# Optimization experiments

Hardware: AMD Instinct MI355X
Metric: run time of the kernel (lower is better)

## Reference

```python
import jax, jax.numpy as jnp
import numpy as np

N_MSB = 4      # bit planes
WB = 8         # weight quant bits
ABNM = 8       # activation quant bits (non-MVM)
NL = 0.1       # noise level


def quant(x, bits, r):
    # quant_pass: symmetric round-to-grid inside [-r, r]
    s = 2.0 ** (bits - 1)
    xs = jnp.clip(x / r, -1.0 + 1.0 / s, 1.0 - 1.0 / s)
    return jnp.round(xs * s) / s * r


def pact(x, a):
    # pact_a reduces to a hard clip to [-a, a]
    return jnp.clip(x, -a, a)


def bitsplit(x, n_msb):
    # x in [0,1] -> n_msb binary planes y[i] and beta weights l2/l1
    l1 = 2.0 ** n_msb - 1.0
    l2 = 2.0 ** (n_msb - 1 - jnp.arange(n_msb, dtype=x.dtype))  # [n_msb]
    y = jnp.floor(jnp.round(l1 * x)[None] / l2[:, None, None]) % 2.0  # [n_msb,B,D]
    return y, l2 / l1


def noisy_bmm(inp, W, b, key):
    # CustomMM_bmm.forward: quantized weights + additive gaussian noise
    kw, kb = jax.random.split(key)
    nw = jax.lax.stop_gradient(jax.random.normal(kw, W.shape, W.dtype) * W.max() * NL)
    nb = jax.lax.stop_gradient(jax.random.normal(kb, b.shape, b.dtype) * b.max() * NL)
    wq = quant(W, WB, 1.0)
    bq = quant(b, WB, 1.0)
    return jnp.einsum('mbi,mio->mbo', inp, wq + nw) + bq + nb  # [n_msb,B,4H]


def setup_inputs() -> dict:
    key = jax.random.key(0)
    ks = jax.random.split(key, 9)
    B, I, H, M = 4096, 256, 1024, N_MSB
    inp = {
        'input': jax.random.normal(ks[0], (B, I), jnp.float32),
        'hx': jax.random.normal(ks[1], (B, H), jnp.float32),
        'cx': jax.random.normal(ks[2], (B, H), jnp.float32),
        'weight_ih': jax.random.normal(ks[3], (M, I, 4 * H), jnp.float32),
        'weight_hh': jax.random.normal(ks[4], (M, H, 4 * H), jnp.float32),
        'bias_ih': jax.random.normal(ks[5], (M, 1, 4 * H), jnp.float32),
        'bias_hh': jax.random.normal(ks[6], (M, 1, 4 * H), jnp.float32),
        'a1': jnp.array([128.0], jnp.float32),
        'a3': jnp.array([1.0], jnp.float32),
        'a4': jnp.array([1.0], jnp.float32),
        'a5': jnp.array([1.0], jnp.float32),
        'a6': jnp.array([1.0], jnp.float32),
        'a7': jnp.array([4.0], jnp.float32),
        'a8': jnp.array([1.0], jnp.float32),
        'a9': jnp.array([4.0], jnp.float32),
        'a10': jnp.array([1.0], jnp.float32),
        'a11': jnp.array([4.0], jnp.float32),
    }
    return inp


def reference(input, hx, cx, weight_ih, weight_hh, bias_ih, bias_hh,
              a1, a3, a4, a5, a6, a7, a8, a9, a10, a11):
    k1, k2 = jax.random.split(jax.random.key(42))
    # input branch: clip -> map to [0,1] -> bit-split -> noisy bmm -> threshold -> beta-sum
    inp01 = (pact(input, a1) + a1) / (a1 * 2)
    y, beta = bitsplit(inp01, N_MSB)
    out = (noisy_bmm(y, weight_ih, bias_ih, k1) > 0.5).astype(input.dtype)
    part1 = (beta[:, None, None] * out).sum(0) * (a1 * 2) - a1
    # hidden branch (note: '+ a1' offset as in the original source)
    inp01 = (pact(hx, a11) + a1) / (a11 * 2)
    y, beta = bitsplit(inp01, N_MSB)
    out = (noisy_bmm(y, weight_hh, bias_hh, k2) > 0.5).astype(input.dtype)
    part2 = (beta[:, None, None] * out).sum(0) * (a11 * 2) - a11
    gates = part1 + part2  # [B, 4H]
    i, j, f, o = jnp.split(gates, 4, axis=1)
    fg = quant(pact(jax.nn.sigmoid(f), a3), ABNM, a3)
    ig = quant(pact(jax.nn.sigmoid(i), a4), ABNM, a4)
    act = quant(pact(jnp.tanh(j), a5), ABNM, a5)
    og = quant(pact(jax.nn.sigmoid(o), a6), ABNM, a6)
    gated_cell = quant(pact(cx * fg, a7), ABNM, a7)
    activated_input = quant(pact(ig * act, a8), ABNM, a8)
    new_c = quant(pact(gated_cell + activated_input, a9), ABNM, a9)
    activated_cell = quant(pact(jnp.tanh(new_c), a10), ABNM, a10)
    new_h = quant(pact(activated_cell * og, a11), ABNM, a11)
    return new_h, new_c
```

## Files before the change

### kernel.cpp

```cpp
#include <hip/hip_runtime.h>
#include <cstdint>
#include <cstddef>


typedef int v4i __attribute__((ext_vector_type(4)));

struct KPc { uint32_t a, b; };

__host__ __device__ constexpr KPc ctf(uint32_t k0, uint32_t k1v, uint32_t c0, uint32_t c1) {
  uint32_t ks2 = k0 ^ k1v ^ 0x1BD11BDAu;
  uint32_t x0 = c0 + k0;
  uint32_t x1 = c1 + k1v;
  uint32_t r0[4] = {13u, 15u, 26u, 6u};
  uint32_t r1[4] = {17u, 29u, 16u, 24u};
  uint32_t ks[3] = {k0, k1v, ks2};
  for (int g = 0; g < 5; ++g) {
    for (int j = 0; j < 4; ++j) {
      uint32_t rr = (g & 1) ? r1[j] : r0[j];
      x0 += x1;
      x1 = (x1 << rr) | (x1 >> (32u - rr));
      x1 ^= x0;
    }
    x0 += ks[(g + 1) % 3];
    x1 += ks[(g + 2) % 3] + (uint32_t)(g + 1);
  }
  return KPc{x0, x1};
}

constexpr KPc K1K  = ctf(0u, 42u, 0u, 0u);
constexpr KPc K2K  = ctf(0u, 42u, 0u, 1u);
constexpr KPc KWIH = ctf(K1K.a, K1K.b, 0u, 0u);
constexpr KPc KBIH = ctf(K1K.a, K1K.b, 0u, 1u);
constexpr KPc KWHH = ctf(K2K.a, K2K.b, 0u, 0u);
constexpr KPc KBHH = ctf(K2K.a, K2K.b, 0u, 1u);

__device__ __forceinline__ uint32_t tf_bits(uint32_t k0, uint32_t k1v, uint32_t j) {
  KPc r = ctf(k0, k1v, 0u, j);
  return r.a ^ r.b;
}

__device__ __forceinline__ unsigned encf(float f) {
  unsigned u = __float_as_uint(f);
  return (u & 0x80000000u) ? ~u : (u | 0x80000000u);
}
__device__ __forceinline__ float decf(unsigned e) {
  unsigned u = (e & 0x80000000u) ? (e & 0x7FFFFFFFu) : ~e;
  return __uint_as_float(u);
}

__global__ void rmax_kernel(const float* __restrict__ x, int n, unsigned* __restrict__ out) {
  unsigned best = 0u;
  for (int i = blockIdx.x * blockDim.x + threadIdx.x; i < n; i += gridDim.x * blockDim.x) {
    unsigned e = encf(x[i]);
    best = best > e ? best : e;
  }
  for (int off = 32; off > 0; off >>= 1) {
    unsigned o = __shfl_down(best, off, 64);
    best = best > o ? best : o;
  }
  __shared__ unsigned sm[4];
  int lane = threadIdx.x & 63, wv = threadIdx.x >> 6;
  if (lane == 0) sm[wv] = best;
  __syncthreads();
  if (threadIdx.x == 0) {
    unsigned b = sm[0];
    for (int i = 1; i < 4; ++i) b = b > sm[i] ? b : sm[i];
    atomicMax(out, b);
  }
}

__device__ __forceinline__ float xla_log1p(float t) {
  float small = __fmul_rn(__fadd_rn(__fmul_rn(-0.5f, t), 1.0f), t);
  float large = logf(__fadd_rn(t, 1.0f));
  return (fabsf(t) < 1e-4f) ? small : large;
}

__device__ __forceinline__ float xla_erfinv(float x) {
  float w = -xla_log1p(-__fmul_rn(x, x));
  float p;
  if (w < 5.0f) {
    float ww = __fadd_rn(w, -2.5f);
    p = 2.81022636e-08f;
    p = __fadd_rn(3.43273939e-07f, __fmul_rn(p, ww));
    p = __fadd_rn(-3.5233877e-06f, __fmul_rn(p, ww));
    p = __fadd_rn(-4.39150654e-06f, __fmul_rn(p, ww));
    p = __fadd_rn(0.00021858087f, __fmul_rn(p, ww));
    p = __fadd_rn(-0.00125372503f, __fmul_rn(p, ww));
    p = __fadd_rn(-0.00417768164f, __fmul_rn(p, ww));
    p = __fadd_rn(0.246640727f, __fmul_rn(p, ww));
    p = __fadd_rn(1.50140941f, __fmul_rn(p, ww));
  } else {
    float ww = __fadd_rn(sqrtf(w), -3.0f);
    p = -0.000200214257f;
    p = __fadd_rn(0.000100950558f, __fmul_rn(p, ww));
    p = __fadd_rn(0.00134934322f, __fmul_rn(p, ww));
    p = __fadd_rn(-0.00367342844f, __fmul_rn(p, ww));
    p = __fadd_rn(0.00573950773f, __fmul_rn(p, ww));
    p = __fadd_rn(-0.0076224613f, __fmul_rn(p, ww));
    p = __fadd_rn(0.00943887047f, __fmul_rn(p, ww));
    p = __fadd_rn(1.00167406f, __fmul_rn(p, ww));
    p = __fadd_rn(2.83297682f, __fmul_rn(p, ww));
  }
  return __fmul_rn(p, x);
}

__device__ __forceinline__ float normal_from_bits(uint32_t bits) {
  float u01 = __uint_as_float((bits >> 9) | 0x3f800000u) - 1.0f;
  const float lo = -0x1.fffffep-1f;
  float u = fmaxf(lo, __fadd_rn(__fmul_rn(u01, 2.0f), lo));
  return __fmul_rn(0x1.6a09e6p+0f, xla_erfinv(u));
}

__device__ __forceinline__ float quantw(float x) {
  float xs = fminf(fmaxf(x, -0.9921875f), 0.9921875f);
  return __fmul_rn(rintf(__fmul_rn(xs, 128.0f)), 0.0078125f);
}

__global__ void gen_t0_kernel(const float* __restrict__ W, float* __restrict__ T0,
                              const unsigned* __restrict__ encp) {
  int j = blockIdx.x * 256 + threadIdx.x;
  if (j >= 1048576) return;
  float wmax = decf(*encp);
  float nrm = normal_from_bits(tf_bits(KWIH.a, KWIH.b, (uint32_t)j));
  float nw = __fmul_rn(__fmul_rn(nrm, wmax), 0.1f);
  T0[j] = __fadd_rn(quantw(W[j]), nw);
}

__global__ void gen_bias_kernel(const float* __restrict__ bsrc, float* __restrict__ bq,
                                float* __restrict__ nb, int n,
                                const unsigned* __restrict__ encp, uint32_t k0, uint32_t k1v) {
  int j = blockIdx.x * 256 + threadIdx.x;
  if (j >= n) return;
  float bmax = decf(*encp);
  float nrm = normal_from_bits(tf_bits(k0, k1v, (uint32_t)j));
  bq[j] = quantw(bsrc[j]);
  nb[j] = __fmul_rn(__fmul_rn(nrm, bmax), 0.1f);
}

__global__ void kv_kernel(const float* __restrict__ x, const float* __restrict__ ap,
                          const float* __restrict__ offp, unsigned char* __restrict__ kvT,
                          int Kdim) {
  int j = blockIdx.x * 256 + threadIdx.x;
  int n = 4096 * Kdim;
  if (j >= n) return;
  int b = j / Kdim, i = j - b * Kdim;
  float a = ap[0], off = offp[0];
  float v = fmaxf(-a, fminf(x[j], a));
  float t = __fdiv_rn(__fadd_rn(v, off), __fmul_rn(a, 2.0f));
  int k = (int)rintf(__fmul_rn(15.0f, t));
  kvT[(size_t)i * 4096 + b] = (unsigned char)(k & 15);
}

__global__ void gen_ahh_kernel(const float* __restrict__ hx, const float* __restrict__ a11p,
                               const float* __restrict__ a1p, signed char* __restrict__ A) {
  int j = blockIdx.x * 256 + threadIdx.x;
  if (j >= 4096 * 1024) return;
  float a = a11p[0], off = a1p[0];
  float v = fmaxf(-a, fminf(hx[j], a));
  float t = __fdiv_rn(__fadd_rn(v, off), __fmul_rn(a, 2.0f));
  int kq = (int)rintf(__fmul_rn(15.0f, t));
  A[j]                      = (signed char)((kq >> 3) & 1);
  A[(size_t)(1 << 22) + j]  = (signed char)((kq >> 2) & 1);
  A[(size_t)(2 << 22) + j]  = (signed char)((kq >> 1) & 1);
  A[(size_t)(3 << 22) + j]  = (signed char)(kq & 1);
}

__global__ void gen_aih_kernel(const float* __restrict__ input, const float* __restrict__ a1p,
                               signed char* __restrict__ A) {
  int j = blockIdx.x * 256 + threadIdx.x;
  if (j >= 4096 * 256) return;
  float a = a1p[0];
  float v = fmaxf(-a, fminf(input[j], a));
  float t = __fdiv_rn(__fadd_rn(v, a), __fmul_rn(a, 2.0f));
  int kq = (int)rintf(__fmul_rn(15.0f, t));
  A[j]                  = (signed char)((kq >> 2) & 1);
  A[1048576 + j]        = (signed char)((kq >> 1) & 1);
  A[2097152 + j]        = (signed char)(kq & 1);
}

__global__ __launch_bounds__(256) void gen_bt_kernel(
    const float* __restrict__ W, signed char* __restrict__ Bt,
    const unsigned* __restrict__ encp, int K, int m0, int nPlanes,
    uint32_t k0k, uint32_t k1k) {
  __shared__ signed char lhi[64 * 68];
  __shared__ signed char llo[64 * 68];
  const int tid = threadIdx.x;
  const int m = m0 + blockIdx.z;
  const int kt = blockIdx.y * 64, ct = blockIdx.x * 64;
  const float wmax = decf(*encp);
#pragma unroll 4
  for (int i = 0; i < 16; ++i) {
    int e = i * 256 + tid;
    int kl = e >> 6, cl = e & 63;
    uint32_t j = (uint32_t)(((m * K + kt + kl) << 12) + ct + cl);
    float nrm = normal_from_bits(tf_bits(k0k, k1k, j));
    float t = __fadd_rn(quantw(W[j]), __fmul_rn(__fmul_rn(nrm, wmax), 0.1f));
    int ti = (int)rintf(__fmul_rn(t, 6144.0f));
    int hi = (ti + 128) >> 8;
    int lo = ti - (hi << 8);
    lhi[cl * 68 + kl] = (signed char)hi;
    llo[cl * 68 + kl] = (signed char)lo;
  }
  __syncthreads();
  const size_t planeElems = (size_t)K << 12;
  signed char* bh = Bt + (size_t)blockIdx.z * planeElems;
  signed char* bl = Bt + (size_t)(nPlanes + blockIdx.z) * planeElems;
#pragma unroll 4
  for (int i = 0; i < 16; ++i) {
    int f = i * 256 + tid;
    int cl = f >> 6, kl = f & 63;
    size_t o = (size_t)(ct + cl) * K + kt + kl;
    bh[o] = lhi[cl * 68 + kl];
    bl[o] = llo[cl * 68 + kl];
  }
}

__global__ __launch_bounds__(256) void gemm_p0_kernel(
    const float* __restrict__ T0, const float* __restrict__ bq, const float* __restrict__ nb,
    const unsigned char* __restrict__ kvT, unsigned char* __restrict__ Kp) {
  const int tid = threadIdx.x, lane = tid & 63, wv = tid >> 6;
  const int c0 = blockIdx.x * 32;
  const int row = blockIdx.y * 256 + wv * 64 + lane;

  float acc[32];
#pragma unroll
  for (int j = 0; j < 32; ++j) acc[j] = 0.0f;

  const unsigned char* kvp = kvT + row;
#pragma unroll 2
  for (int k = 0; k < 256; ++k) {
    unsigned nib = kvp[(size_t)k << 12];
    float f = (float)((nib >> 3) & 1u);
    const float4* tp = (const float4*)(T0 + ((size_t)k << 12) + c0);
    float4 tv[8];
#pragma unroll
    for (int q = 0; q < 8; ++q) tv[q] = tp[q];
#pragma unroll
    for (int q = 0; q < 8; ++q) {
      acc[q * 4 + 0] = __builtin_fmaf(f, tv[q].x, acc[q * 4 + 0]);
      acc[q * 4 + 1] = __builtin_fmaf(f, tv[q].y, acc[q * 4 + 1]);
      acc[q * 4 + 2] = __builtin_fmaf(f, tv[q].z, acc[q * 4 + 2]);
      acc[q * 4 + 3] = __builtin_fmaf(f, tv[q].w, acc[q * 4 + 3]);
    }
  }

#pragma unroll
  for (int j = 0; j < 32; ++j) {
    int col = c0 + j;
    float s = __fadd_rn(__fadd_rn(acc[j], bq[col]), nb[col]);
    Kp[((size_t)row << 12) + col] = (s > 0.5f) ? (unsigned char)8 : (unsigned char)0;
  }
}

typedef __attribute__((address_space(3))) signed char lds_i8;
typedef __attribute__((address_space(1))) const signed char g_i8;

__device__ __forceinline__ void glds16(const signed char* g, signed char* l) {
  __builtin_amdgcn_global_load_lds((g_i8*)g, (lds_i8*)l, 16, 0, 0);
}

__global__ __launch_bounds__(256, 3) void gemm_mfma_kernel(
    const signed char* __restrict__ Ahh, const signed char* __restrict__ Bthh,
    const signed char* __restrict__ Aih, const signed char* __restrict__ Btih,
    const float* __restrict__ bqh, const float* __restrict__ nbh,
    const float* __restrict__ bqi, const float* __restrict__ nbi,
    unsigned char* __restrict__ Kp) {
  const int tid = threadIdx.x;
  const int lane = tid & 63, wv = tid >> 6;
  const int col0 = blockIdx.x * 64;
  const int row0 = blockIdx.y * 128;
  const int wrow = (wv >> 1) * 64;
  const int wcol = (wv & 1) * 32;

  __shared__ __align__(16) signed char smbuf[2][16384];
  const int HOFF = 8192, LOFF = 12288;

  const int l15 = lane & 15;
  const int cc  = (((lane >> 4) ^ ((lane >> 1) & 3)) << 4);
  const int xq  = ((((lane & 3) ^ ((lane >> 3) & 3))) << 4);
  const int lr  = lane >> 2;

  uint32_t k12[4][2];
#pragma unroll
  for (int rf = 0; rf < 4; ++rf) { k12[rf][0] = 0u; k12[rf][1] = 0u; }

  for (int sub = 0; sub < 7; ++sub) {
    int K, w;
    const signed char *A, *Bh, *Bl;
    const float *bqp, *nbp;
    if (sub < 4) {
      int m = sub;
      K = 1024;
      A  = Ahh  + ((size_t)m << 22);
      Bh = Bthh + ((size_t)m << 22);
      Bl = Bthh + ((size_t)(4 + m) << 22);
      bqp = bqh + (m << 12); nbp = nbh + (m << 12);
      w = (1 << (3 - m)) << 4;
    } else {
      int m = sub - 3;
      K = 256;
      A  = Aih  + ((size_t)(m - 1) << 20);
      Bh = Btih + ((size_t)(m - 1) << 20);
      Bl = Btih + ((size_t)(3 + m - 1) << 20);
      bqp = bqi + (m << 12); nbp = nbi + (m << 12);
      w = 1 << (3 - m);
    }

    const size_t soff = (size_t)lr * K + xq;
    const signed char* gA  = A  + (size_t)(row0 + 32 * wv) * K + soff;
    const signed char* gA2 = gA + (size_t)16 * K;
    const signed char* gH  = Bh + (size_t)(col0 + 16 * wv) * K + soff;
    const signed char* gL  = Bl + (size_t)(col0 + 16 * wv) * K + soff;

    auto stage = [&](int cb, int k0) {
      signed char* base = &smbuf[cb][0];
      glds16(gA  + k0, base + (32 * wv) * 64);
      glds16(gA2 + k0, base + (32 * wv + 16) * 64);
      glds16(gH  + k0, base + HOFF + (16 * wv) * 64);
      glds16(gL  + k0, base + LOFF + (16 * wv) * 64);
    };

    v4i ach[4][2], acl[4][2];
    v4i zero = {0, 0, 0, 0};
#pragma unroll
    for (int rf = 0; rf < 4; ++rf)
#pragma unroll
      for (int cf = 0; cf < 2; ++cf) { ach[rf][cf] = zero; acl[rf][cf] = zero; }

    int cur = 0;
    stage(0, 0);
    __syncthreads();

    const int nt = K >> 6;
    for (int t = 0; t < nt; ++t) {
      if (t + 1 < nt) stage(cur ^ 1, (t + 1) << 6);

      const signed char* bb = &smbuf[cur][0];
      v4i af[4], bfh[2], bfl[2];
#pragma unroll
      for (int rf = 0; rf < 4; ++rf)
        af[rf] = *(const v4i*)(bb + (wrow + rf * 16 + l15) * 64 + cc);
#pragma unroll
      for (int cf = 0; cf < 2; ++cf) {
        bfh[cf] = *(const v4i*)(bb + HOFF + (wcol + cf * 16 + l15) * 64 + cc);
        bfl[cf] = *(const v4i*)(bb + LOFF + (wcol + cf * 16 + l15) * 64 + cc);
      }
#pragma unroll
      for (int rf = 0; rf < 4; ++rf)
#pragma unroll
        for (int cf = 0; cf < 2; ++cf) {
          ach[rf][cf] = __builtin_amdgcn_mfma_i32_16x16x64_i8(af[rf], bfh[cf], ach[rf][cf], 0, 0, 0);
          acl[rf][cf] = __builtin_amdgcn_mfma_i32_16x16x64_i8(af[rf], bfl[cf], acl[rf][cf], 0, 0, 0);
        }
      __syncthreads();
      cur ^= 1;
    }

#pragma unroll
    for (int cf = 0; cf < 2; ++cf) {
      int col = col0 + wcol + cf * 16 + l15;
      float bqc = bqp[col];
      float nbc = nbp[col];
#pragma unroll
      for (int rf = 0; rf < 4; ++rf)
#pragma unroll
        for (int r = 0; r < 4; ++r) {
          int tot = ach[rf][cf][r] * 256 + acl[rf][cf][r];
          float s = __fmul_rn((float)tot, (1.0f / 6144.0f));
          float s2 = __fadd_rn(__fadd_rn(s, bqc), nbc);
          if (s2 > 0.5f) k12[rf][cf] += ((uint32_t)w << (8 * r));
        }
    }
  }

#pragma unroll
  for (int rf = 0; rf < 4; ++rf)
#pragma unroll
    for (int cf = 0; cf < 2; ++cf)
#pragma unroll
      for (int r = 0; r < 4; ++r) {
        int row = row0 + wrow + rf * 16 + ((lane >> 4) << 2) + r;
        int col = col0 + wcol + cf * 16 + l15;
        size_t o = ((size_t)row << 12) + col;
        Kp[o] = (unsigned char)(Kp[o] | ((k12[rf][cf] >> (8 * r)) & 255u));
      }
}

__device__ __forceinline__ float quant8(float x, float r) {
  float xs = __fdiv_rn(x, r);
  xs = fminf(fmaxf(xs, -0.9921875f), 0.9921875f);
  float q = rintf(__fmul_rn(xs, 128.0f));
  return __fmul_rn(__fdiv_rn(q, 128.0f), r);
}
__device__ __forceinline__ float pactf(float x, float a) { return fminf(fmaxf(x, -a), a); }
__device__ __forceinline__ double sigd(double x) { return 1.0 / (1.0 + exp(-x)); }

__global__ void tail_kernel(const unsigned char* __restrict__ Kp, const float* __restrict__ cx,
                            const float* a1p, const float* a3p, const float* a4p,
                            const float* a5p, const float* a6p, const float* a7p,
                            const float* a8p, const float* a9p, const float* a10p,
                            const float* a11p, float* __restrict__ out) {
  int idx = blockIdx.x * 256 + threadIdx.x;
  if (idx >= 4096 * 1024) return;
  int b = idx >> 10, h = idx & 1023;
  double a1 = (double)a1p[0], a11 = (double)a11p[0];
  const unsigned char* row = Kp + (size_t)b * 4096 + h;
  int pI = row[0], pJ = row[1024], pF = row[2048], pO = row[3072];
  auto gate = [&](int pk) -> double {
    double s1 = (double)(pk & 15) * (1.0 / 15.0);
    double s2 = (double)(pk >> 4) * (1.0 / 15.0);
    return (s1 * (2.0 * a1) - a1) + (s2 * (2.0 * a11) - a11);
  };
  double gi = gate(pI), gj = gate(pJ), gf = gate(pF), go = gate(pO);
  float a3 = a3p[0], a4 = a4p[0], a5 = a5p[0], a6 = a6p[0];
  float a7 = a7p[0], a8 = a8p[0], a9 = a9p[0], a10 = a10p[0], a11f = a11p[0];
  float fg  = quant8(pactf((float)sigd(gf), a3), a3);
  float ig  = quant8(pactf((float)sigd(gi), a4), a4);
  float act = quant8(pactf((float)tanh(gj), a5), a5);
  float og  = quant8(pactf((float)sigd(go), a6), a6);
  float cxv = cx[idx];
  float gc  = quant8(pactf(__fmul_rn(cxv, fg), a7), a7);
  float ai  = quant8(pactf(__fmul_rn(ig, act), a8), a8);
  float nc  = quant8(pactf(__fadd_rn(gc, ai), a9), a9);
  float ac  = quant8(pactf((float)tanh((double)nc), a10), a10);
  float nh  = quant8(pactf(__fmul_rn(ac, og), a11f), a11f);
  out[idx] = nh;
  out[4194304 + idx] = nc;
}

extern "C" void kernel_launch(void* const* d_in, const int* in_sizes, int n_in,
                              void* d_out, int out_size, void* d_ws, size_t ws_size,
                              hipStream_t stream) {
  const float* input = (const float*)d_in[0];
  const float* hx    = (const float*)d_in[1];
  const float* cx    = (const float*)d_in[2];
  const float* wih   = (const float*)d_in[3];
  const float* whh   = (const float*)d_in[4];
  const float* bih   = (const float*)d_in[5];
  const float* bhh   = (const float*)d_in[6];
  const float* a1p   = (const float*)d_in[7];
  const float* a3p   = (const float*)d_in[8];
  const float* a4p   = (const float*)d_in[9];
  const float* a5p   = (const float*)d_in[10];
  const float* a6p   = (const float*)d_in[11];
  const float* a7p   = (const float*)d_in[12];
  const float* a8p   = (const float*)d_in[13];
  const float* a9p   = (const float*)d_in[14];
  const float* a10p  = (const float*)d_in[15];
  const float* a11p  = (const float*)d_in[16];

  char* ws = (char*)d_ws;
  unsigned* enc        = (unsigned*)ws;
  float* T0            = (float*)(ws + 256);
  float* bq_ih         = (float*)(ws + 256 + 4194304);
  float* nb_ih         = bq_ih + 16384;
  float* bq_hh         = nb_ih + 16384;
  float* nb_hh         = bq_hh + 16384;
  unsigned char* kv_ih = (unsigned char*)(nb_hh + 16384);
  signed char* A_hh    = (signed char*)(kv_ih + 1048576);
  signed char* Bt_hh   = A_hh + 16777216;
  signed char* A_ih    = Bt_hh + 33554432;
  signed char* Bt_ih   = A_ih + 3145728;
  unsigned char* Kp    = (unsigned char*)(Bt_ih + 6291456);

  hipMemsetAsync(enc, 0, 64, stream);
  rmax_kernel<<<512, 256, 0, stream>>>(wih, 4 * 256 * 4096, enc + 0);
  rmax_kernel<<<512, 256, 0, stream>>>(whh, 4 * 1024 * 4096, enc + 1);
  rmax_kernel<<<64, 256, 0, stream>>>(bih, 16384, enc + 2);
  rmax_kernel<<<64, 256, 0, stream>>>(bhh, 16384, enc + 3);

  kv_kernel<<<4096, 256, 0, stream>>>(input, a1p, a1p, kv_ih, 256);
  gen_aih_kernel<<<4096, 256, 0, stream>>>(input, a1p, A_ih);
  gen_ahh_kernel<<<16384, 256, 0, stream>>>(hx, a11p, a1p, A_hh);

  gen_bias_kernel<<<64, 256, 0, stream>>>(bih, bq_ih, nb_ih, 16384, enc + 2, KBIH.a, KBIH.b);
  gen_bias_kernel<<<64, 256, 0, stream>>>(bhh, bq_hh, nb_hh, 16384, enc + 3, KBHH.a, KBHH.b);

  gen_t0_kernel<<<4096, 256, 0, stream>>>(wih, T0, enc + 0);
  gen_bt_kernel<<<dim3(64, 16, 4), 256, 0, stream>>>(whh, Bt_hh, enc + 1, 1024, 0, 4,
                                                     KWHH.a, KWHH.b);
  gen_bt_kernel<<<dim3(64, 4, 3), 256, 0, stream>>>(wih, Bt_ih, enc + 0, 256, 1, 3,
                                                    KWIH.a, KWIH.b);

  gemm_p0_kernel<<<dim3(128, 16), 256, 0, stream>>>(T0, bq_ih, nb_ih, kv_ih, Kp);
  gemm_mfma_kernel<<<dim3(64, 32), 256, 0, stream>>>(A_hh, Bt_hh, A_ih, Bt_ih,
                                                     bq_hh, nb_hh, bq_ih, nb_ih, Kp);

  tail_kernel<<<16384, 256, 0, stream>>>(Kp, cx, a1p, a3p, a4p, a5p, a6p, a7p, a8p, a9p,
                                         a10p, a11p, (float*)d_out);
}
```

Measured before the change: 676.3 us.

## Triple-buffer MFMA GEMM loads with single barrier and tile kv transpose via LDS

The int8 MFMA GEMM moves from a double-buffered LDS pipeline with two barriers per k-step to a three-buffer ring. It prefetches two tiles ahead and uses explicit vmcnt waits plus one barrier per iteration, so global-to-LDS loads overlap more with MFMA work. Separately, kv_kernel now transposes through a 64x64 shared tile so both its global reads and writes are coalesced, replacing scattered byte stores. The third buffer raises LDS use to 48KB per block, which may reduce occupancy under the launch bound of 3 blocks.

Measured after the change: 673.6 us. No clear change (-0.4%).

```diff
diff --git a/kernel.cpp b/kernel.cpp
--- a/kernel.cpp
+++ b/kernel.cpp
@@ -137,18 +137,29 @@
   nb[j] = __fmul_rn(__fmul_rn(nrm, bmax), 0.1f);
 }
 
-__global__ void kv_kernel(const float* __restrict__ x, const float* __restrict__ ap,
-                          const float* __restrict__ offp, unsigned char* __restrict__ kvT,
-                          int Kdim) {
-  int j = blockIdx.x * 256 + threadIdx.x;
-  int n = 4096 * Kdim;
-  if (j >= n) return;
-  int b = j / Kdim, i = j - b * Kdim;
-  float a = ap[0], off = offp[0];
-  float v = fmaxf(-a, fminf(x[j], a));
-  float t = __fdiv_rn(__fadd_rn(v, off), __fmul_rn(a, 2.0f));
-  int k = (int)rintf(__fmul_rn(15.0f, t));
-  kvT[(size_t)i * 4096 + b] = (unsigned char)(k & 15);
+__global__ __launch_bounds__(256) void kv_kernel(
+    const float* __restrict__ x, const float* __restrict__ ap,
+    const float* __restrict__ offp, unsigned char* __restrict__ kvT, int Kdim) {
+  __shared__ unsigned char tile[64][65];
+  const int tid = threadIdx.x;
+  const int bt = blockIdx.x * 64, it = blockIdx.y * 64;
+  const float a = ap[0], off = offp[0];
+#pragma unroll
+  for (int e = 0; e < 16; ++e) {
+    int idx = e * 256 + tid;
+    int bl = idx >> 6, il = idx & 63;
+    float v = fmaxf(-a, fminf(x[(size_t)(bt + bl) * Kdim + it + il], a));
+    float t = __fdiv_rn(__fadd_rn(v, off), __fmul_rn(a, 2.0f));
+    int k = (int)rintf(__fmul_rn(15.0f, t));
+    tile[il][bl] = (unsigned char)(k & 15);
+  }
+  __syncthreads();
+#pragma unroll
+  for (int e = 0; e < 16; ++e) {
+    int idx = e * 256 + tid;
+    int il = idx >> 6, bl = idx & 63;
+    kvT[(size_t)(it + il) * 4096 + bt + bl] = tile[il][bl];
+  }
 }
 
 __global__ void gen_ahh_kernel(const float* __restrict__ hx, const float* __restrict__ a11p,
@@ -272,7 +283,7 @@
   const int wrow = (wv >> 1) * 64;
   const int wcol = (wv & 1) * 32;
 
-  __shared__ __align__(16) signed char smbuf[2][16384];
+  __shared__ __align__(16) signed char smbuf[3][16384];
   const int HOFF = 8192, LOFF = 12288;
 
   const int l15 = lane & 15;
@@ -312,8 +323,7 @@
     const signed char* gH  = Bh + (size_t)(col0 + 16 * wv) * K + soff;
     const signed char* gL  = Bl + (size_t)(col0 + 16 * wv) * K + soff;
 
-    auto stage = [&](int cb, int k0) {
-      signed char* base = &smbuf[cb][0];
+    auto stage = [&](signed char* base, int k0) {
       glds16(gA  + k0, base + (32 * wv) * 64);
       glds16(gA2 + k0, base + (32 * wv + 16) * 64);
       glds16(gH  + k0, base + HOFF + (16 * wv) * 64);
@@ -327,23 +337,32 @@
 #pragma unroll
       for (int cf = 0; cf < 2; ++cf) { ach[rf][cf] = zero; acl[rf][cf] = zero; }
 
-    int cur = 0;
-    stage(0, 0);
-    __syncthreads();
+    signed char* bc = &smbuf[0][0];
+    signed char* bn = &smbuf[1][0];
+    signed char* bf = &smbuf[2][0];
 
     const int nt = K >> 6;
+    stage(bc, 0);
+    stage(bn, 64);
+
     for (int t = 0; t < nt; ++t) {
-      if (t + 1 < nt) stage(cur ^ 1, (t + 1) << 6);
-
-      const signed char* bb = &smbuf[cur][0];
+      if (t + 1 < nt) {
+        asm volatile("s_waitcnt vmcnt(4)" ::: "memory");
+      } else {
+        asm volatile("s_waitcnt vmcnt(0)" ::: "memory");
+      }
+      __builtin_amdgcn_s_barrier();
+      __builtin_amdgcn_sched_barrier(0);
+      if (t + 2 < nt) stage(bf, (t + 2) << 6);
+
       v4i af[4], bfh[2], bfl[2];
 #pragma unroll
       for (int rf = 0; rf < 4; ++rf)
-        af[rf] = *(const v4i*)(bb + (wrow + rf * 16 + l15) * 64 + cc);
+        af[rf] = *(const v4i*)(bc + (wrow + rf * 16 + l15) * 64 + cc);
 #pragma unroll
       for (int cf = 0; cf < 2; ++cf) {
-        bfh[cf] = *(const v4i*)(bb + HOFF + (wcol + cf * 16 + l15) * 64 + cc);
-        bfl[cf] = *(const v4i*)(bb + LOFF + (wcol + cf * 16 + l15) * 64 + cc);
+        bfh[cf] = *(const v4i*)(bc + HOFF + (wcol + cf * 16 + l15) * 64 + cc);
+        bfl[cf] = *(const v4i*)(bc + LOFF + (wcol + cf * 16 + l15) * 64 + cc);
       }
 #pragma unroll
       for (int rf = 0; rf < 4; ++rf)
@@ -352,9 +371,9 @@
           ach[rf][cf] = __builtin_amdgcn_mfma_i32_16x16x64_i8(af[rf], bfh[cf], ach[rf][cf], 0, 0, 0);
           acl[rf][cf] = __builtin_amdgcn_mfma_i32_16x16x64_i8(af[rf], bfl[cf], acl[rf][cf], 0, 0, 0);
         }
-      __syncthreads();
-      cur ^= 1;
+      signed char* tmp = bc; bc = bn; bn = bf; bf = tmp;
     }
+    __syncthreads();
 
 #pragma unroll
     for (int cf = 0; cf < 2; ++cf) {
@@ -469,7 +488,7 @@
   rmax_kernel<<<64, 256, 0, stream>>>(bih, 16384, enc + 2);
   rmax_kernel<<<64, 256, 0, stream>>>(bhh, 16384, enc + 3);
 
-  kv_kernel<<<4096, 256, 0, stream>>>(input, a1p, a1p, kv_ih, 256);
+  kv_kernel<<<dim3(64, 4), 256, 0, stream>>>(input, a1p, a1p, kv_ih, 256);
   gen_aih_kernel<<<4096, 256, 0, stream>>>(input, a1p, A_ih);
   gen_ahh_kernel<<<16384, 256, 0, stream>>>(hx, a11p, a1p, A_hh);
 
```
